# Performance work log

Measured on AMD Instinct MI355X. Metric: run time of the kernel, lower is better.

Reference implementation:

```python
import jax, jax.numpy as jnp
import numpy as np

N = 2_097_152
EPS = 1e-6


def _tri(x):
    # triangleWave (period 2), maps R -> [0, 1]; applied to 'normalize=True' tables
    return 2.0 * jnp.abs(x / 2.0 - jnp.floor(x / 2.0 + 0.5))


def _grid2d(uv, table, bilinear, normalize):
    # uv: (N,2) in [0,1); table: (U,V,L)
    t = _tri(table) if normalize else table
    U, V, _ = t.shape
    u = jnp.clip(uv[:, 0], 0.0, 1.0 - EPS) * (U - 1)
    v = jnp.clip(uv[:, 1], 0.0, 1.0 - EPS) * (V - 1)
    if bilinear:
        u0 = jnp.floor(u)
        v0 = jnp.floor(v)
        fu = (u - u0)[:, None]
        fv = (v - v0)[:, None]
        u0i = u0.astype(jnp.int32)
        v0i = v0.astype(jnp.int32)
        u1i = jnp.minimum(u0i + 1, U - 1)
        v1i = jnp.minimum(v0i + 1, V - 1)
        return (t[u0i, v0i] * (1 - fu) * (1 - fv)
                + t[u1i, v0i] * fu * (1 - fv)
                + t[u0i, v1i] * (1 - fu) * fv
                + t[u1i, v1i] * fu * fv)
    return t[jnp.round(u).astype(jnp.int32), jnp.round(v).astype(jnp.int32)]


def _grid1d(u, table, bilinear, normalize):
    # u: (N,) in [0,1); table: (U,L)
    t = _tri(table) if normalize else table
    U, _ = t.shape
    uu = jnp.clip(u, 0.0, 1.0 - EPS) * (U - 1)
    if bilinear:
        u0 = jnp.floor(uu)
        fu = (uu - u0)[:, None]
        u0i = u0.astype(jnp.int32)
        u1i = jnp.minimum(u0i + 1, U - 1)
        return t[u0i] * (1 - fu) + t[u1i] * fu
    return t[jnp.round(uu).astype(jnp.int32)]


def setup_inputs() -> dict:
    key = jax.random.key(0)
    ks = jax.random.split(key, 17)
    mk = lambda i, shape: jax.random.uniform(ks[i], shape, dtype=jnp.float32)
    names = ["roughNoh", "anisoToh", "nDotLV", "tDotLV", "metalLoh",
             "subCg", "spst", "shst", "lumCs"]
    d = {n: mk(i, (N, 2)) for i, n in enumerate(names)}
    d["tabRAEnc"] = mk(9, (2048, 2048, 2))
    d["tabCgEnc"] = mk(10, (2048, 1))
    d["tabRSEnc"] = mk(11, (64, 64, 3))
    d["tabRADec"] = mk(12, (48, 48, 3))
    d["tabCgDec"] = mk(13, (96, 2))
    d["tabLVR"] = mk(14, (32, 32, 1))
    d["tabLV"] = mk(15, (32, 32, 4))
    d["tabNHL"] = mk(16, (32, 32, 4))
    return d


def reference(roughNoh, anisoToh, nDotLV, tDotLV, metalLoh, subCg, spst, shst,
              lumCs, tabRAEnc, tabCgEnc, tabRSEnc, tabRADec, tabCgDec,
              tabLVR, tabLV, tabNHL):
    raIn = jnp.stack((roughNoh[:, 0], anisoToh[:, 0]), axis=1)  # (N,2)
    metallicity = metalLoh[:, 0]
    # ---- encoder: LUT lookups + elementwise mixing coefficients ----
    ra = _grid2d(raIn, tabRAEnc, bilinear=False, normalize=True)           # (N,2)
    cg = _grid1d(subCg[:, 1], tabCgEnc, bilinear=False, normalize=True)    # (N,1)
    rsEnc = _grid2d(jnp.concatenate((raIn[:, 0:1], subCg[:, 0:1]), axis=1),
                    tabRSEnc, bilinear=True, normalize=True)               # (N,3)
    cd = (1 - metallicity) * lumCs[:, 0]
    cm0 = (spst[:, 0] * 0.1 * (1 - metallicity) * spst[:, 1]
           + metallicity * lumCs[:, 0])[:, None]
    cm1 = (spst[:, 0] * 0.1 * (1 - metallicity) * (1 - spst[:, 1]))[:, None]
    cs0 = (shst[:, 0] * (1 - metallicity) * shst[:, 1])[:, None]
    cs1 = (shst[:, 0] * (1 - metallicity) * (1 - shst[:, 1]))[:, None]
    cc = (0.25 * 0.25 * lumCs[:, 1])[:, None]
    rsCd = rsEnc * cd[:, None]                                             # (N,3)
    # ---- decoder LUTs ----
    raCoefs = _grid2d(ra, tabRADec, bilinear=True, normalize=False)        # (N,3)
    cgCoefs = _grid1d(cg[:, 0], tabCgDec, bilinear=True, normalize=False)  # (N,2)
    vTerm = _grid2d(jnp.concatenate((nDotLV[:, 0:1] * nDotLV[:, 1:2],
                                     ra[:, 0:1]), axis=1),
                    tabLVR, bilinear=True, normalize=True)                 # (N,1)
    nlvCoefs = _grid2d(nDotLV, tabLV, bilinear=True, normalize=True)       # (N,4)
    nhlCoefs = _grid2d(jnp.stack((metalLoh[:, 1], nDotLV[:, 0]), axis=1),
                       tabNHL, bilinear=True, normalize=True)              # (N,4)
    # ---- elementwise shading combination ----
    noh2 = roughNoh[:, 1] ** 2
    den = raCoefs[:, 0] * anisoToh[:, 1] ** 2 + raCoefs[:, 1] * noh2 + raCoefs[:, 2]
    dTerm = (0.25 / (nDotLV[:, 1] * den ** 2))[:, None]
    x = (rsCd[:, 0:1] * metalLoh[:, 1:2] * nlvCoefs[:, 1:2]
         + rsCd[:, 1:2] * nlvCoefs[:, 2:3]
         + rsCd[:, 2:3] * nlvCoefs[:, 3:4]
         + cm0 * vTerm * nhlCoefs[:, 2:3] * dTerm
         + cs0 * nhlCoefs[:, 0:1])
    y = (((1 - cm1) * nhlCoefs[:, 3:4] + cm1) * vTerm * dTerm
         + cs1 * nhlCoefs[:, 0:1]
         + cc * nhlCoefs[:, 1:2] * nlvCoefs[:, 0:1]
           / (nDotLV[:, 1] * (cgCoefs[:, 0] * noh2 + cgCoefs[:, 1]))[:, None])
    return jnp.concatenate((x, y), axis=1)  # (N,2)
```

## Files before the change

### kernel.cpp

```cpp
#include <hip/hip_runtime.h>
#include <hip/hip_fp16.h>

#define CLIP_HI (1.0f - 1e-6f)

typedef float f4v __attribute__((ext_vector_type(4)));

__device__ __forceinline__ float tri_(float x) {
    return 2.0f * fabsf(x * 0.5f - floorf(x * 0.5f + 0.5f));
}

__device__ __forceinline__ float clamp01(float x) {
    return fminf(fmaxf(x, 0.0f), CLIP_HI);
}

__device__ __forceinline__ float4 nt_load4(const float* p) {
    f4v v = __builtin_nontemporal_load((const f4v*)p);
    return make_float4(v.x, v.y, v.z, v.w);
}
__device__ __forceinline__ void nt_store4(float* p, float4 v) {
    f4v t = {v.x, v.y, v.z, v.w};
    __builtin_nontemporal_store(t, (f4v*)p);
}

struct H4 { __half2 xy, zw; };

struct BW {
    int i00, i10, i01, i11;
    float w00, w10, w01, w11;
};

template <int U, int V>
__device__ __forceinline__ BW bw2d(float uc, float vc) {
    float u = clamp01(uc) * (float)(U - 1);
    float v = clamp01(vc) * (float)(V - 1);
    float u0f = floorf(u), v0f = floorf(v);
    float fu = u - u0f, fv = v - v0f;
    int u0 = (int)u0f, v0 = (int)v0f;
    BW r;
    r.i00 = u0 * V + v0;
    r.i10 = r.i00 + V;
    r.i01 = r.i00 + 1;
    r.i11 = r.i10 + 1;
    float gu = 1.0f - fu, gv = 1.0f - fv;
    r.w00 = gu * gv; r.w10 = fu * gv; r.w01 = gu * fv; r.w11 = fu * fv;
    return r;
}

__device__ __forceinline__ float4 h4_blend(H4 A, H4 B, H4 C, H4 D, const BW& b) {
    float2 Axy = __half22float2(A.xy), Azw = __half22float2(A.zw);
    float2 Bxy = __half22float2(B.xy), Bzw = __half22float2(B.zw);
    float2 Cxy = __half22float2(C.xy), Czw = __half22float2(C.zw);
    float2 Dxy = __half22float2(D.xy), Dzw = __half22float2(D.zw);
    return make_float4(
        Axy.x * b.w00 + Bxy.x * b.w10 + Cxy.x * b.w01 + Dxy.x * b.w11,
        Axy.y * b.w00 + Bxy.y * b.w10 + Cxy.y * b.w01 + Dxy.y * b.w11,
        Azw.x * b.w00 + Bzw.x * b.w10 + Czw.x * b.w01 + Dzw.x * b.w11,
        Azw.y * b.w00 + Bzw.y * b.w10 + Czw.y * b.w01 + Dzw.y * b.w11);
}

__device__ __forceinline__ float3 blend3(const __half2* tAB, const __half* tC,
                                         const BW& b) {
    float2 A = __half22float2(tAB[b.i00]);
    float2 B = __half22float2(tAB[b.i10]);
    float2 C = __half22float2(tAB[b.i01]);
    float2 D = __half22float2(tAB[b.i11]);
    float3 r;
    r.x = A.x * b.w00 + B.x * b.w10 + C.x * b.w01 + D.x * b.w11;
    r.y = A.y * b.w00 + B.y * b.w10 + C.y * b.w01 + D.y * b.w11;
    r.z = __half2float(tC[b.i00]) * b.w00 + __half2float(tC[b.i10]) * b.w10 +
          __half2float(tC[b.i01]) * b.w01 + __half2float(tC[b.i11]) * b.w11;
    return r;
}

__global__ __launch_bounds__(256) void prep_kernel(const float* __restrict__ t_rs,
                                                   const float* __restrict__ t_cge,
                                                   const float* __restrict__ t_cgd,
                                                   __half2* __restrict__ o_rsAB,
                                                   __half* __restrict__ o_rsC,
                                                   __half2* __restrict__ o_cg) {
    int j = blockIdx.x * 256 + threadIdx.x;
    if (j < 64 * 64) {
        float a = tri_(t_rs[j * 3 + 0]);
        float b = tri_(t_rs[j * 3 + 1]);
        float c = tri_(t_rs[j * 3 + 2]);
        o_rsAB[j] = __floats2half2_rn(a, b);
        o_rsC[j]  = __float2half(c);
    }
    if (j < 2048) {
        float cg = tri_(t_cge[j]);
        float u = clamp01(cg) * 95.0f;
        float u0f = floorf(u);
        float fu = u - u0f;
        int u0 = (int)u0f;
        int u1 = min(u0 + 1, 95);
        float2 a = ((const float2*)t_cgd)[u0];
        float2 b = ((const float2*)t_cgd)[u1];
        o_cg[j] = __floats2half2_rn(a.x * (1.0f - fu) + b.x * fu,
                                    a.y * (1.0f - fu) + b.y * fu);
    }
}

__device__ __forceinline__ float2 gatherRA(const float* __restrict__ tabRAEnc,
                                           float rNx, float aTx) {
    int ui = (int)rintf(clamp01(rNx) * 2047.0f);
    int vi = (int)rintf(clamp01(aTx) * 2047.0f);
    return ((const float2*)tabRAEnc)[ui * 2048 + vi];
}

template <bool USE_WS>
__device__ __forceinline__ float2 shadeB(
    float rNx, float rNy, float aTy, float nLVx, float nLVy,
    float mLx, float mLy, float sCx, float sCy, float spx, float spy,
    float shx, float shy, float lCx, float lCy,
    float2 raT,
    const __half2* __restrict__ cgComp,
    const float* __restrict__ tabCgEnc, const float* __restrict__ tabCgDec,
    const __half2* sRsAB, const __half* sRsC,
    const __half2* sRadAB, const __half* sRadC,
    const __half* sLVR, const H4* sLV, const H4* sNHL)
{
    float rs0, rs1, rs2;
    {
        BW b = bw2d<64, 64>(rNx, sCx);
        float3 r = blend3(sRsAB, sRsC, b);
        rs0 = r.x; rs1 = r.y; rs2 = r.z;
    }

    float2 cgC;
    {
        int ci = (int)rintf(clamp01(sCy) * 2047.0f);
        if constexpr (USE_WS) {
            cgC = __half22float2(cgComp[ci]);
        } else {
            float cg = tri_(tabCgEnc[ci]);
            float u = clamp01(cg) * 95.0f;
            float u0f = floorf(u);
            float fu = u - u0f;
            int u0 = (int)u0f;
            int u1 = min(u0 + 1, 95);
            float2 a = ((const float2*)tabCgDec)[u0];
            float2 b = ((const float2*)tabCgDec)[u1];
            cgC = make_float2(a.x * (1.0f - fu) + b.x * fu,
                              a.y * (1.0f - fu) + b.y * fu);
        }
    }

    float4 nlv, nhl;
    {
        BW b = bw2d<32, 32>(nLVx, nLVy);
        nlv = h4_blend(sLV[b.i00], sLV[b.i10], sLV[b.i01], sLV[b.i11], b);
    }
    {
        BW b = bw2d<32, 32>(mLy, nLVx);
        nhl = h4_blend(sNHL[b.i00], sNHL[b.i10], sNHL[b.i01], sNHL[b.i11], b);
    }

    float ra0 = tri_(raT.x);
    float ra1 = tri_(raT.y);

    float raC0, raC1, raC2;
    {
        BW b = bw2d<48, 48>(ra0, ra1);
        float3 r = blend3(sRadAB, sRadC, b);
        raC0 = r.x; raC1 = r.y; raC2 = r.z;
    }

    float vTerm;
    {
        BW b = bw2d<32, 32>(nLVx * nLVy, ra0);
        vTerm = __half2float(sLVR[b.i00]) * b.w00 + __half2float(sLVR[b.i10]) * b.w10 +
                __half2float(sLVR[b.i01]) * b.w01 + __half2float(sLVR[b.i11]) * b.w11;
    }

    float met = mLx;
    float om  = 1.0f - met;
    float cd  = om * lCx;
    float cm0 = spx * 0.1f * om * spy + met * lCx;
    float cm1 = spx * 0.1f * om * (1.0f - spy);
    float cs0 = shx * om * shy;
    float cs1 = shx * om * (1.0f - shy);
    float cc  = 0.0625f * lCy;

    float noh2 = rNy * rNy;
    float den  = raC0 * aTy * aTy + raC1 * noh2 + raC2;
    float dTerm = 0.25f / (nLVy * den * den);

    float x = rs0 * cd * mLy * nlv.y + rs1 * cd * nlv.z + rs2 * cd * nlv.w
            + cm0 * vTerm * nhl.z * dTerm + cs0 * nhl.x;

    float y = ((1.0f - cm1) * nhl.w + cm1) * vTerm * dTerm
            + cs1 * nhl.x
            + cc * nhl.y * nlv.x / (nLVy * (cgC.x * noh2 + cgC.y));

    return make_float2(x, y);
}

template <bool USE_WS>
__global__ __launch_bounds__(512, 4) void disney_main(
    const float* __restrict__ roughNoh,
    const float* __restrict__ anisoToh,
    const float* __restrict__ nDotLV,
    const float* __restrict__ metalLoh,
    const float* __restrict__ subCg,
    const float* __restrict__ spst,
    const float* __restrict__ shst,
    const float* __restrict__ lumCs,
    const float* __restrict__ tabRAEnc,
    const float* __restrict__ tabCgEnc,
    const float* __restrict__ tabCgDec,
    const float* __restrict__ tabRSEnc,
    const float* __restrict__ tabRADec,
    const __half2* __restrict__ wsRsAB,
    const __half*  __restrict__ wsRsC,
    const __half2* __restrict__ cgComp,
    const float* __restrict__ tabLVR,
    const float* __restrict__ tabLV,
    const float* __restrict__ tabNHL,
    float* __restrict__ out,
    int n)
{
    __shared__ __half2 sRsAB[4096];
    __shared__ __half  sRsC [4096];
    __shared__ __half2 sRadAB[2304];
    __shared__ __half  sRadC [2304];
    __shared__ __half  sLVR[1024];
    __shared__ H4      sLV [1024];
    __shared__ H4      sNHL[1024];

    int tid = threadIdx.x;

#pragma unroll
    for (int k = 0; k < 8; ++k) {
        int j = tid + k * 512;
        if constexpr (USE_WS) {
            sRsAB[j] = wsRsAB[j];
            sRsC[j]  = wsRsC[j];
        } else {
            float a = tri_(tabRSEnc[j * 3 + 0]);
            float b = tri_(tabRSEnc[j * 3 + 1]);
            float c = tri_(tabRSEnc[j * 3 + 2]);
            sRsAB[j] = __floats2half2_rn(a, b);
            sRsC[j]  = __float2half(c);
        }
    }
    for (int j = tid; j < 2304; j += 512) {
        sRadAB[j] = __floats2half2_rn(tabRADec[j * 3 + 0], tabRADec[j * 3 + 1]);
        sRadC[j]  = __float2half(tabRADec[j * 3 + 2]);
    }
#pragma unroll
    for (int k = 0; k < 2; ++k) {
        int j = tid + k * 512;
        sLVR[j] = __float2half(tri_(tabLVR[j]));
        float4 v = ((const float4*)tabLV)[j];
        H4 h; h.xy = __floats2half2_rn(tri_(v.x), tri_(v.y));
              h.zw = __floats2half2_rn(tri_(v.z), tri_(v.w));
        sLV[j] = h;
        float4 w = ((const float4*)tabNHL)[j];
        H4 h2; h2.xy = __floats2half2_rn(tri_(w.x), tri_(w.y));
               h2.zw = __floats2half2_rn(tri_(w.z), tri_(w.w));
        sNHL[j] = h2;
    }
    __syncthreads();

    int P = (n + 1) >> 1;
    int H = (P + 1) >> 1;
    int t = blockIdx.x * 512 + tid;
    if (t >= H) return;
    int p1 = t;
    int p2 = t + H;

    bool full1 = (2 * p1 + 1) < n;
    bool full2 = (p2 < P) && ((2 * p2 + 1) < n);

    if (full1 && full2) {
        float4 rN1 = nt_load4(roughNoh + 4 * p1);
        float4 aT1 = nt_load4(anisoToh + 4 * p1);
        float4 rN2 = nt_load4(roughNoh + 4 * p2);
        float4 aT2 = nt_load4(anisoToh + 4 * p2);

        float2 raT0 = gatherRA(tabRAEnc, rN1.x, aT1.x);
        float2 raT1 = gatherRA(tabRAEnc, rN1.z, aT1.z);
        float2 raT2 = gatherRA(tabRAEnc, rN2.x, aT2.x);
        float2 raT3 = gatherRA(tabRAEnc, rN2.z, aT2.z);

        float4 nLV1 = nt_load4(nDotLV   + 4 * p1);
        float4 mL1  = nt_load4(metalLoh + 4 * p1);
        float4 sC1  = nt_load4(subCg    + 4 * p1);
        float4 sp1  = nt_load4(spst     + 4 * p1);
        float4 sh1  = nt_load4(shst     + 4 * p1);
        float4 lC1  = nt_load4(lumCs    + 4 * p1);
        float4 nLV2 = nt_load4(nDotLV   + 4 * p2);
        float4 mL2  = nt_load4(metalLoh + 4 * p2);
        float4 sC2  = nt_load4(subCg    + 4 * p2);
        float4 sp2  = nt_load4(spst     + 4 * p2);
        float4 sh2  = nt_load4(shst     + 4 * p2);
        float4 lC2  = nt_load4(lumCs    + 4 * p2);

        float2 r0 = shadeB<USE_WS>(rN1.x, rN1.y, aT1.y, nLV1.x, nLV1.y,
                                   mL1.x, mL1.y, sC1.x, sC1.y, sp1.x, sp1.y,
                                   sh1.x, sh1.y, lC1.x, lC1.y, raT0,
                                   cgComp, tabCgEnc, tabCgDec,
                                   sRsAB, sRsC, sRadAB, sRadC,
                                   sLVR, sLV, sNHL);
        float2 r1 = shadeB<USE_WS>(rN1.z, rN1.w, aT1.w, nLV1.z, nLV1.w,
                                   mL1.z, mL1.w, sC1.z, sC1.w, sp1.z, sp1.w,
                                   sh1.z, sh1.w, lC1.z, lC1.w, raT1,
                                   cgComp, tabCgEnc, tabCgDec,
                                   sRsAB, sRsC, sRadAB, sRadC,
                                   sLVR, sLV, sNHL);
        nt_store4(out + 4 * p1, make_float4(r0.x, r0.y, r1.x, r1.y));

        float2 r2 = shadeB<USE_WS>(rN2.x, rN2.y, aT2.y, nLV2.x, nLV2.y,
                                   mL2.x, mL2.y, sC2.x, sC2.y, sp2.x, sp2.y,
                                   sh2.x, sh2.y, lC2.x, lC2.y, raT2,
                                   cgComp, tabCgEnc, tabCgDec,
                                   sRsAB, sRsC, sRadAB, sRadC,
                                   sLVR, sLV, sNHL);
        float2 r3 = shadeB<USE_WS>(rN2.z, rN2.w, aT2.w, nLV2.z, nLV2.w,
                                   mL2.z, mL2.w, sC2.z, sC2.w, sp2.z, sp2.w,
                                   sh2.z, sh2.w, lC2.z, lC2.w, raT3,
                                   cgComp, tabCgEnc, tabCgDec,
                                   sRsAB, sRsC, sRadAB, sRadC,
                                   sLVR, sLV, sNHL);
        nt_store4(out + 4 * p2, make_float4(r2.x, r2.y, r3.x, r3.y));
    } else {
        int es[4] = { 2 * p1, 2 * p1 + 1,
                      (p2 < P) ? 2 * p2 : n, (p2 < P) ? 2 * p2 + 1 : n };
#pragma unroll
        for (int k = 0; k < 4; ++k) {
            int e = es[k];
            if (e >= n) continue;
            float2 rN  = ((const float2*)roughNoh)[e];
            float2 aT  = ((const float2*)anisoToh)[e];
            float2 nLV = ((const float2*)nDotLV)[e];
            float2 mL  = ((const float2*)metalLoh)[e];
            float2 sC  = ((const float2*)subCg)[e];
            float2 sp  = ((const float2*)spst)[e];
            float2 sh  = ((const float2*)shst)[e];
            float2 lC  = ((const float2*)lumCs)[e];
            float2 raT = gatherRA(tabRAEnc, rN.x, aT.x);
            float2 r = shadeB<USE_WS>(rN.x, rN.y, aT.y, nLV.x, nLV.y,
                                      mL.x, mL.y, sC.x, sC.y, sp.x, sp.y,
                                      sh.x, sh.y, lC.x, lC.y, raT,
                                      cgComp, tabCgEnc, tabCgDec,
                                      sRsAB, sRsC, sRadAB, sRadC,
                                      sLVR, sLV, sNHL);
            ((float2*)out)[e] = r;
        }
    }
}

extern "C" void kernel_launch(void* const* d_in, const int* in_sizes, int n_in,
                              void* d_out, int out_size, void* d_ws, size_t ws_size,
                              hipStream_t stream) {
    const float* roughNoh = (const float*)d_in[0];
    const float* anisoToh = (const float*)d_in[1];
    const float* nDotLV   = (const float*)d_in[2];
    const float* metalLoh = (const float*)d_in[4];
    const float* subCg    = (const float*)d_in[5];
    const float* spst     = (const float*)d_in[6];
    const float* shst     = (const float*)d_in[7];
    const float* lumCs    = (const float*)d_in[8];
    const float* tabRAEnc = (const float*)d_in[9];
    const float* tabCgEnc = (const float*)d_in[10];
    const float* tabRSEnc = (const float*)d_in[11];
    const float* tabRADec = (const float*)d_in[12];
    const float* tabCgDec = (const float*)d_in[13];
    const float* tabLVR   = (const float*)d_in[14];
    const float* tabLV    = (const float*)d_in[15];
    const float* tabNHL   = (const float*)d_in[16];

    int n = in_sizes[0] / 2;
    float* out = (float*)d_out;

    const int block = 512;
    int P = (n + 1) / 2;
    int H = (P + 1) / 2;
    int grid = (H + block - 1) / block;

    const size_t OFF_RSC = 4096 * sizeof(__half2);
    const size_t OFF_CG  = OFF_RSC + 4096 * sizeof(__half);
    const size_t WS_NEED = OFF_CG + 2048 * sizeof(__half2);
    bool use_ws = ws_size >= WS_NEED;
    __half2* ws_rsAB = (__half2*)d_ws;
    __half*  ws_rsC  = (__half*)((char*)d_ws + OFF_RSC);
    __half2* ws_cg   = (__half2*)((char*)d_ws + OFF_CG);

    if (use_ws) {
        prep_kernel<<<(64 * 64 + 255) / 256, 256, 0, stream>>>(
            tabRSEnc, tabCgEnc, tabCgDec, ws_rsAB, ws_rsC, ws_cg);
        disney_main<true><<<grid, block, 0, stream>>>(
            roughNoh, anisoToh, nDotLV, metalLoh, subCg, spst, shst, lumCs,
            tabRAEnc, tabCgEnc, tabCgDec, tabRSEnc, tabRADec,
            ws_rsAB, ws_rsC, ws_cg,
            tabLVR, tabLV, tabNHL, out, n);
    } else {
        disney_main<false><<<grid, block, 0, stream>>>(
            roughNoh, anisoToh, nDotLV, metalLoh, subCg, spst, shst, lumCs,
            tabRAEnc, tabCgEnc, tabCgDec, tabRSEnc, tabRADec,
            ws_rsAB, ws_rsC, ws_cg,
            tabLVR, tabLV, tabNHL, out, n);
    }
}
```

Measured before the change: 227.1 us.

## Move RADec third channel to global half table and process one pair per thread

The third channel of the RADec decode table no longer lives in shared memory. It is precomputed to a half-precision global workspace by the prep kernel, and in the fallback path it is read straight from the float table. This shrinks LDS use per block. Each thread now handles one element pair instead of two, which doubles the grid and cuts per-thread register pressure and per-block table-load amortization. The exchange is four uncached-in-LDS global gathers per element for that channel, plus more blocks that each repeat the shared-table fill.

New measurement: 233.9 us. +3.0%, slower.

```diff
diff --git a/kernel.cpp b/kernel.cpp
--- a/kernel.cpp
+++ b/kernel.cpp
@@ -75,9 +75,11 @@
 __global__ __launch_bounds__(256) void prep_kernel(const float* __restrict__ t_rs,
                                                    const float* __restrict__ t_cge,
                                                    const float* __restrict__ t_cgd,
+                                                   const float* __restrict__ t_rad,
                                                    __half2* __restrict__ o_rsAB,
                                                    __half* __restrict__ o_rsC,
-                                                   __half2* __restrict__ o_cg) {
+                                                   __half2* __restrict__ o_cg,
+                                                   __half* __restrict__ o_radC) {
     int j = blockIdx.x * 256 + threadIdx.x;
     if (j < 64 * 64) {
         float a = tri_(t_rs[j * 3 + 0]);
@@ -98,6 +100,9 @@
         o_cg[j] = __floats2half2_rn(a.x * (1.0f - fu) + b.x * fu,
                                     a.y * (1.0f - fu) + b.y * fu);
     }
+    if (j < 2304) {
+        o_radC[j] = __float2half(t_rad[j * 3 + 2]);
+    }
 }
 
 __device__ __forceinline__ float2 gatherRA(const float* __restrict__ tabRAEnc,
@@ -115,8 +120,9 @@
     float2 raT,
     const __half2* __restrict__ cgComp,
     const float* __restrict__ tabCgEnc, const float* __restrict__ tabCgDec,
+    const __half* __restrict__ gRadC, const float* __restrict__ tabRADec,
     const __half2* sRsAB, const __half* sRsC,
-    const __half2* sRadAB, const __half* sRadC,
+    const __half2* sRadAB,
     const __half* sLVR, const H4* sLV, const H4* sNHL)
 {
     float rs0, rs1, rs2;
@@ -161,8 +167,19 @@
     float raC0, raC1, raC2;
     {
         BW b = bw2d<48, 48>(ra0, ra1);
-        float3 r = blend3(sRadAB, sRadC, b);
-        raC0 = r.x; raC1 = r.y; raC2 = r.z;
+        float2 A = __half22float2(sRadAB[b.i00]);
+        float2 B = __half22float2(sRadAB[b.i10]);
+        float2 C = __half22float2(sRadAB[b.i01]);
+        float2 D = __half22float2(sRadAB[b.i11]);
+        raC0 = A.x * b.w00 + B.x * b.w10 + C.x * b.w01 + D.x * b.w11;
+        raC1 = A.y * b.w00 + B.y * b.w10 + C.y * b.w01 + D.y * b.w11;
+        if constexpr (USE_WS) {
+            raC2 = __half2float(gRadC[b.i00]) * b.w00 + __half2float(gRadC[b.i10]) * b.w10 +
+                   __half2float(gRadC[b.i01]) * b.w01 + __half2float(gRadC[b.i11]) * b.w11;
+        } else {
+            raC2 = tabRADec[b.i00 * 3 + 2] * b.w00 + tabRADec[b.i10 * 3 + 2] * b.w10 +
+                   tabRADec[b.i01 * 3 + 2] * b.w01 + tabRADec[b.i11 * 3 + 2] * b.w11;
+        }
     }
 
     float vTerm;
@@ -213,6 +230,7 @@
     const __half2* __restrict__ wsRsAB,
     const __half*  __restrict__ wsRsC,
     const __half2* __restrict__ cgComp,
+    const __half*  __restrict__ gRadC,
     const float* __restrict__ tabLVR,
     const float* __restrict__ tabLV,
     const float* __restrict__ tabNHL,
@@ -222,7 +240,6 @@
     __shared__ __half2 sRsAB[4096];
     __shared__ __half  sRsC [4096];
     __shared__ __half2 sRadAB[2304];
-    __shared__ __half  sRadC [2304];
     __shared__ __half  sLVR[1024];
     __shared__ H4      sLV [1024];
     __shared__ H4      sNHL[1024];
@@ -245,7 +262,6 @@
     }
     for (int j = tid; j < 2304; j += 512) {
         sRadAB[j] = __floats2half2_rn(tabRADec[j * 3 + 0], tabRADec[j * 3 + 1]);
-        sRadC[j]  = __float2half(tabRADec[j * 3 + 2]);
     }
 #pragma unroll
     for (int k = 0; k < 2; ++k) {
@@ -263,72 +279,38 @@
     __syncthreads();
 
     int P = (n + 1) >> 1;
-    int H = (P + 1) >> 1;
-    int t = blockIdx.x * 512 + tid;
-    if (t >= H) return;
-    int p1 = t;
-    int p2 = t + H;
-
-    bool full1 = (2 * p1 + 1) < n;
-    bool full2 = (p2 < P) && ((2 * p2 + 1) < n);
-
-    if (full1 && full2) {
-        float4 rN1 = nt_load4(roughNoh + 4 * p1);
-        float4 aT1 = nt_load4(anisoToh + 4 * p1);
-        float4 rN2 = nt_load4(roughNoh + 4 * p2);
-        float4 aT2 = nt_load4(anisoToh + 4 * p2);
-
-        float2 raT0 = gatherRA(tabRAEnc, rN1.x, aT1.x);
-        float2 raT1 = gatherRA(tabRAEnc, rN1.z, aT1.z);
-        float2 raT2 = gatherRA(tabRAEnc, rN2.x, aT2.x);
-        float2 raT3 = gatherRA(tabRAEnc, rN2.z, aT2.z);
-
-        float4 nLV1 = nt_load4(nDotLV   + 4 * p1);
-        float4 mL1  = nt_load4(metalLoh + 4 * p1);
-        float4 sC1  = nt_load4(subCg    + 4 * p1);
-        float4 sp1  = nt_load4(spst     + 4 * p1);
-        float4 sh1  = nt_load4(shst     + 4 * p1);
-        float4 lC1  = nt_load4(lumCs    + 4 * p1);
-        float4 nLV2 = nt_load4(nDotLV   + 4 * p2);
-        float4 mL2  = nt_load4(metalLoh + 4 * p2);
-        float4 sC2  = nt_load4(subCg    + 4 * p2);
-        float4 sp2  = nt_load4(spst     + 4 * p2);
-        float4 sh2  = nt_load4(shst     + 4 * p2);
-        float4 lC2  = nt_load4(lumCs    + 4 * p2);
-
-        float2 r0 = shadeB<USE_WS>(rN1.x, rN1.y, aT1.y, nLV1.x, nLV1.y,
-                                   mL1.x, mL1.y, sC1.x, sC1.y, sp1.x, sp1.y,
-                                   sh1.x, sh1.y, lC1.x, lC1.y, raT0,
-                                   cgComp, tabCgEnc, tabCgDec,
-                                   sRsAB, sRsC, sRadAB, sRadC,
-                                   sLVR, sLV, sNHL);
-        float2 r1 = shadeB<USE_WS>(rN1.z, rN1.w, aT1.w, nLV1.z, nLV1.w,
-                                   mL1.z, mL1.w, sC1.z, sC1.w, sp1.z, sp1.w,
-                                   sh1.z, sh1.w, lC1.z, lC1.w, raT1,
-                                   cgComp, tabCgEnc, tabCgDec,
-                                   sRsAB, sRsC, sRadAB, sRadC,
-                                   sLVR, sLV, sNHL);
-        nt_store4(out + 4 * p1, make_float4(r0.x, r0.y, r1.x, r1.y));
-
-        float2 r2 = shadeB<USE_WS>(rN2.x, rN2.y, aT2.y, nLV2.x, nLV2.y,
-                                   mL2.x, mL2.y, sC2.x, sC2.y, sp2.x, sp2.y,
-                                   sh2.x, sh2.y, lC2.x, lC2.y, raT2,
-                                   cgComp, tabCgEnc, tabCgDec,
-                                   sRsAB, sRsC, sRadAB, sRadC,
-                                   sLVR, sLV, sNHL);
-        float2 r3 = shadeB<USE_WS>(rN2.z, rN2.w, aT2.w, nLV2.z, nLV2.w,
-                                   mL2.z, mL2.w, sC2.z, sC2.w, sp2.z, sp2.w,
-                                   sh2.z, sh2.w, lC2.z, lC2.w, raT3,
-                                   cgComp, tabCgEnc, tabCgDec,
-                                   sRsAB, sRsC, sRadAB, sRadC,
-                                   sLVR, sLV, sNHL);
-        nt_store4(out + 4 * p2, make_float4(r2.x, r2.y, r3.x, r3.y));
+    int p = blockIdx.x * 512 + tid;
+    if (p >= P) return;
+
+    if (2 * p + 1 < n) {
+        float4 rN = nt_load4(roughNoh + 4 * p);
+        float4 aT = nt_load4(anisoToh + 4 * p);
+
+        float2 raT0 = gatherRA(tabRAEnc, rN.x, aT.x);
+        float2 raT1 = gatherRA(tabRAEnc, rN.z, aT.z);
+
+        float4 nLV = nt_load4(nDotLV   + 4 * p);
+        float4 mL  = nt_load4(metalLoh + 4 * p);
+        float4 sC  = nt_load4(subCg    + 4 * p);
+        float4 sp  = nt_load4(spst     + 4 * p);
+        float4 sh  = nt_load4(shst     + 4 * p);
+        float4 lC  = nt_load4(lumCs    + 4 * p);
+
+        float2 r0 = shadeB<USE_WS>(rN.x, rN.y, aT.y, nLV.x, nLV.y,
+                                   mL.x, mL.y, sC.x, sC.y, sp.x, sp.y,
+                                   sh.x, sh.y, lC.x, lC.y, raT0,
+                                   cgComp, tabCgEnc, tabCgDec, gRadC, tabRADec,
+                                   sRsAB, sRsC, sRadAB, sLVR, sLV, sNHL);
+        float2 r1 = shadeB<USE_WS>(rN.z, rN.w, aT.w, nLV.z, nLV.w,
+                                   mL.z, mL.w, sC.z, sC.w, sp.z, sp.w,
+                                   sh.z, sh.w, lC.z, lC.w, raT1,
+                                   cgComp, tabCgEnc, tabCgDec, gRadC, tabRADec,
+                                   sRsAB, sRsC, sRadAB, sLVR, sLV, sNHL);
+        nt_store4(out + 4 * p, make_float4(r0.x, r0.y, r1.x, r1.y));
     } else {
-        int es[4] = { 2 * p1, 2 * p1 + 1,
-                      (p2 < P) ? 2 * p2 : n, (p2 < P) ? 2 * p2 + 1 : n };
 #pragma unroll
-        for (int k = 0; k < 4; ++k) {
-            int e = es[k];
+        for (int k = 0; k < 2; ++k) {
+            int e = 2 * p + k;
             if (e >= n) continue;
             float2 rN  = ((const float2*)roughNoh)[e];
             float2 aT  = ((const float2*)anisoToh)[e];
@@ -342,9 +324,8 @@
             float2 r = shadeB<USE_WS>(rN.x, rN.y, aT.y, nLV.x, nLV.y,
                                       mL.x, mL.y, sC.x, sC.y, sp.x, sp.y,
                                       sh.x, sh.y, lC.x, lC.y, raT,
-                                      cgComp, tabCgEnc, tabCgDec,
-                                      sRsAB, sRsC, sRadAB, sRadC,
-                                      sLVR, sLV, sNHL);
+                                      cgComp, tabCgEnc, tabCgDec, gRadC, tabRADec,
+                                      sRsAB, sRsC, sRadAB, sLVR, sLV, sNHL);
             ((float2*)out)[e] = r;
         }
     }
@@ -375,30 +356,32 @@
 
     const int block = 512;
     int P = (n + 1) / 2;
-    int H = (P + 1) / 2;
-    int grid = (H + block - 1) / block;
-
-    const size_t OFF_RSC = 4096 * sizeof(__half2);
-    const size_t OFF_CG  = OFF_RSC + 4096 * sizeof(__half);
-    const size_t WS_NEED = OFF_CG + 2048 * sizeof(__half2);
+    int grid = (P + block - 1) / block;
+
+    const size_t OFF_RSC  = 4096 * sizeof(__half2);
+    const size_t OFF_CG   = OFF_RSC + 4096 * sizeof(__half);
+    const size_t OFF_RADC = OFF_CG + 2048 * sizeof(__half2);
+    const size_t WS_NEED  = OFF_RADC + 2304 * sizeof(__half);
     bool use_ws = ws_size >= WS_NEED;
     __half2* ws_rsAB = (__half2*)d_ws;
     __half*  ws_rsC  = (__half*)((char*)d_ws + OFF_RSC);
     __half2* ws_cg   = (__half2*)((char*)d_ws + OFF_CG);
+    __half*  ws_radC = (__half*)((char*)d_ws + OFF_RADC);
 
     if (use_ws) {
         prep_kernel<<<(64 * 64 + 255) / 256, 256, 0, stream>>>(
-            tabRSEnc, tabCgEnc, tabCgDec, ws_rsAB, ws_rsC, ws_cg);
+            tabRSEnc, tabCgEnc, tabCgDec, tabRADec,
+            ws_rsAB, ws_rsC, ws_cg, ws_radC);
         disney_main<true><<<grid, block, 0, stream>>>(
             roughNoh, anisoToh, nDotLV, metalLoh, subCg, spst, shst, lumCs,
             tabRAEnc, tabCgEnc, tabCgDec, tabRSEnc, tabRADec,
-            ws_rsAB, ws_rsC, ws_cg,
+            ws_rsAB, ws_rsC, ws_cg, ws_radC,
             tabLVR, tabLV, tabNHL, out, n);
     } else {
         disney_main<false><<<grid, block, 0, stream>>>(
             roughNoh, anisoToh, nDotLV, metalLoh, subCg, spst, shst, lumCs,
             tabRAEnc, tabCgEnc, tabCgDec, tabRSEnc, tabRADec,
-            ws_rsAB, ws_rsC, ws_cg,
+            ws_rsAB, ws_rsC, ws_cg, ws_radC,
             tabLVR, tabLV, tabNHL, out, n);
     }
 }
```
